# Performance work log

Hardware: AMD Instinct MI355X
Metric: run time of the kernel (lower is better)

## Reference

```python
import jax, jax.numpy as jnp
import numpy as np
import math

N_TOTAL = 262144
C = 128
B = 512
LMAX = 512  # max segment length (static for jit)


def setup_inputs() -> dict:
    key = jax.random.key(0)
    ks = jax.random.split(key, 8)
    Q_feature = jax.random.normal(ks[0], (N_TOTAL, C), dtype=jnp.float32)
    K_feature = jax.random.normal(ks[1], (N_TOTAL, C), dtype=jnp.float32)
    # cumulative offsets: equal segments of length LMAX (general code handles ragged)
    offset = (jnp.arange(1, B + 1, dtype=jnp.int64) * (N_TOTAL // B))
    s = 1.0 / math.sqrt(C)
    Wq = jax.random.normal(ks[2], (C, C), dtype=jnp.float32) * s
    Wk = jax.random.normal(ks[3], (C, C), dtype=jnp.float32) * s
    Wv = jax.random.normal(ks[4], (C, C), dtype=jnp.float32) * s
    bq = jnp.zeros((C,), dtype=jnp.float32)
    bk = jnp.zeros((C,), dtype=jnp.float32)
    bv = jnp.zeros((C,), dtype=jnp.float32)
    return {"Q_feature": Q_feature, "K_feature": K_feature,
            "Wq": Wq, "bq": bq, "Wk": Wk, "bk": bk, "Wv": Wv, "bv": bv,
            "offset": offset}


def reference(Q_feature, K_feature, Wq, bq, Wk, bk, Wv, bv, offset):
    N, Cdim = Q_feature.shape
    Q = Q_feature @ Wq.T + bq
    K = K_feature @ Wk.T + bk
    V = K_feature @ Wv.T + bv

    starts = jnp.concatenate([jnp.zeros((1,), offset.dtype), offset[:-1]])
    lengths = offset - starts                         # (B,)
    pos = jnp.arange(LMAX)                            # (LMAX,)
    idx = jnp.clip(starts[:, None] + pos[None, :], 0, N - 1)  # (B, LMAX)
    mask = pos[None, :] < lengths[:, None]            # (B, LMAX) valid tokens

    Qp = Q[idx]                                       # (B, LMAX, C)
    Kp = K[idx]
    Vp = V[idx]

    scale = 1.0 / math.sqrt(Cdim)
    scores = jnp.einsum('blc,bmc->blm', Qp, Kp) * scale     # (B, LMAX, LMAX)
    scores = jnp.where(mask[:, None, :], scores, jnp.float32(-1e30))
    attn = jax.nn.softmax(scores, axis=-1)
    outp = jnp.einsum('blm,bmc->blc', attn, Vp)             # (B, LMAX, C)
    outp = outp * mask[:, :, None]                          # zero padded rows

    # scatter padded segments back to flat (N, C); idx is an exact partition on valid rows
    out = jnp.zeros((N, Cdim), dtype=outp.dtype).at[idx].add(outp)
    return out
```

## Files before the change

### kernel.cpp

```cpp
#include <hip/hip_runtime.h>
#include <hip/hip_bf16.h>

#define CDIM 128
#define LMAXC 512
#define QBLK 128
#define KVBLK 64

#define QSCALE (0.08838834764831845f * 1.4426950408889634f)

typedef __attribute__((ext_vector_type(8))) short bf16x8;
typedef __attribute__((ext_vector_type(4))) short bf16x4;
typedef __attribute__((ext_vector_type(4))) float f32x4;

__device__ inline short f2bf(float f) {
    union { float f; unsigned u; } v; v.f = f;
    unsigned r = v.u + 0x7FFFu + ((v.u >> 16) & 1u);
    return (short)(r >> 16);
}

__device__ inline bf16x8 cvt8v(float4 a, float4 b) {
    bf16x8 o;
    o[0] = f2bf(a.x); o[1] = f2bf(a.y); o[2] = f2bf(a.z); o[3] = f2bf(a.w);
    o[4] = f2bf(b.x); o[5] = f2bf(b.y); o[6] = f2bf(b.z); o[7] = f2bf(b.w);
    return o;
}

__device__ inline unsigned pk2(float lo, float hi) {
    unsigned r;
    asm("v_cvt_pk_bf16_f32 %0, %1, %2" : "=v"(r) : "v"(lo), "v"(hi));
    return r;
}

__device__ inline void gload16(const void* g, void* l) {
    __builtin_amdgcn_global_load_lds(
        (const __attribute__((address_space(1))) unsigned*)g,
        (__attribute__((address_space(3))) unsigned*)l, 16, 0, 0);
}

__device__ inline void blk_barrier() {
    __builtin_amdgcn_sched_barrier(0);
    __builtin_amdgcn_s_barrier();
    __builtin_amdgcn_sched_barrier(0);
}

__device__ inline int pch(int q) { return ((q + (q >> 3)) & 7) << 4; }

__global__ void wcvt_kernel(const float* __restrict__ Wq,
                            const float* __restrict__ Wk,
                            const float* __restrict__ Wv,
                            short* __restrict__ Wbf)
{
    int t = blockIdx.x * 256 + threadIdx.x;
    int m = t / 2048;
    int e = (t % 2048) * 8;
    const float* W = (m == 0) ? Wq : (m == 1) ? Wk : Wv;
    float sc = (m == 0) ? QSCALE : 1.0f;
    float4 a = *reinterpret_cast<const float4*>(W + e);
    float4 b = *reinterpret_cast<const float4*>(W + e + 4);
    a.x *= sc; a.y *= sc; a.z *= sc; a.w *= sc;
    b.x *= sc; b.y *= sc; b.z *= sc; b.w *= sc;
    *reinterpret_cast<bf16x8*>(Wbf + m * 16384 + e) = cvt8v(a, b);
}

__device__ inline void tile_qk(const char* __restrict__ wlds,
                               const bf16x8 xfr[2][4],
                               const float* __restrict__ bias, float bsc,
                               short* __restrict__ outp, int rowb,
                               int lrow, int lhalf)
{
#pragma unroll
    for (int cf = 0; cf < 8; ++cf) {
        const int key = cf * 16 + lrow;
        bf16x8 wfr[4];
#pragma unroll
        for (int ks = 0; ks < 4; ++ks) {
            int wb = (key * 256 + (ks * 32 + lhalf * 8) * 2) ^ ((key & 7) << 4);
            wfr[ks] = *reinterpret_cast<const bf16x8*>(wlds + wb);
        }
        float4 bv4 = *reinterpret_cast<const float4*>(bias + cf * 16 + lhalf * 4);
#pragma unroll
        for (int xt = 0; xt < 2; ++xt) {
            f32x4 acc = {0.f, 0.f, 0.f, 0.f};
#pragma unroll
            for (int ks = 0; ks < 4; ++ks)
                acc = __builtin_amdgcn_mfma_f32_16x16x32_bf16(wfr[ks], xfr[xt][ks], acc, 0, 0, 0);
            bf16x4 pk;
            pk[0] = f2bf(acc[0] + bv4.x * bsc);
            pk[1] = f2bf(acc[1] + bv4.y * bsc);
            pk[2] = f2bf(acc[2] + bv4.z * bsc);
            pk[3] = f2bf(acc[3] + bv4.w * bsc);
            *reinterpret_cast<bf16x4*>(
                outp + (size_t)(rowb + xt * 16 + lrow) * CDIM
                     + cf * 16 + lhalf * 4) = pk;
        }
    }
}

__device__ inline void tile_v(const char* __restrict__ wlds,
                              const bf16x8 xfr[2][4],
                              const float* __restrict__ bv,
                              short* __restrict__ Vt, int rowb, int N,
                              int lrow, int lhalf)
{
#pragma unroll
    for (int cf = 0; cf < 8; ++cf) {
        const int d = cf * 16 + lrow;
        bf16x8 wfr[4];
#pragma unroll
        for (int ks = 0; ks < 4; ++ks) {
            int wb = (d * 256 + (ks * 32 + lhalf * 8) * 2) ^ ((d & 7) << 4);
            wfr[ks] = *reinterpret_cast<const bf16x8*>(wlds + wb);
        }
        f32x4 acc0 = {0.f, 0.f, 0.f, 0.f};
        f32x4 acc1 = {0.f, 0.f, 0.f, 0.f};
#pragma unroll
        for (int ks = 0; ks < 4; ++ks) {
            acc0 = __builtin_amdgcn_mfma_f32_16x16x32_bf16(xfr[0][ks], wfr[ks], acc0, 0, 0, 0);
            acc1 = __builtin_amdgcn_mfma_f32_16x16x32_bf16(xfr[1][ks], wfr[ks], acc1, 0, 0, 0);
        }
        float bcol = bv[d];
        bf16x4 p0, p1;
#pragma unroll
        for (int r = 0; r < 4; ++r) {
            p0[r] = f2bf(acc0[r] + bcol);
            p1[r] = f2bf(acc1[r] + bcol);
        }
        short* vrow = Vt + (size_t)d * N + rowb + lhalf * 4;
        *reinterpret_cast<bf16x4*>(vrow)      = p0;
        *reinterpret_cast<bf16x4*>(vrow + 16) = p1;
    }
}

__global__ __launch_bounds__(512) void projkv_kernel(
    const float* __restrict__ Kf, const short* __restrict__ Wbf,
    const float* __restrict__ bk, const float* __restrict__ bv,
    short* __restrict__ Kp, short* __restrict__ Vt, int N)
{
    __shared__ __align__(16) char wlds[32768];

    const int tid   = threadIdx.x;
    const int lane  = tid & 63;
    const int wv    = tid >> 6;
    const int lrow  = lane & 15;
    const int lhalf = lane >> 4;
    const int rowb  = blockIdx.x * 256 + wv * 32;

#pragma unroll
    for (int j = 0; j < 4; ++j) {
        int beta = j * 8192 + tid * 16;
        int r  = beta >> 8;
        int gs = ((beta >> 4) & 15) ^ (r & 7);
        gload16(Wbf + 16384 + r * 128 + gs * 8, wlds + beta);
    }

    bf16x8 xfr[2][4];
#pragma unroll
    for (int xt = 0; xt < 2; ++xt) {
        const float* xr = Kf + (size_t)(rowb + xt * 16 + lrow) * CDIM + lhalf * 8;
#pragma unroll
        for (int ks = 0; ks < 4; ++ks) {
            const float4* s = reinterpret_cast<const float4*>(xr + ks * 32);
            xfr[xt][ks] = cvt8v(s[0], s[1]);
        }
    }
    __syncthreads();

    tile_qk(wlds, xfr, bk, 1.0f, Kp, rowb, lrow, lhalf);
    __syncthreads();
#pragma unroll
    for (int j = 0; j < 4; ++j) {
        int beta = j * 8192 + tid * 16;
        int r  = beta >> 8;
        int gs = ((beta >> 4) & 15) ^ (r & 7);
        gload16(Wbf + 32768 + r * 128 + gs * 8, wlds + beta);
    }
    __syncthreads();
    tile_v(wlds, xfr, bv, Vt, rowb, N, lrow, lhalf);
}

__global__ __launch_bounds__(256) void attn_kernel(
    const float* __restrict__ Qf, const short* __restrict__ Wbf,
    const float* __restrict__ bq,
    const short* __restrict__ Kp, const short* __restrict__ VtG,
    const int* __restrict__ offset, float* __restrict__ out, int Ntot)
{
    __shared__ __align__(16) char smem[81920];
    char* lds_p = smem + 65536;

    const int nq = LMAXC / QBLK;
    int flat = blockIdx.x, total = gridDim.x;
    int seg, qb;
    if ((total & (8 * nq - 1)) == 0) {
        int per = total >> 3;
        int xcd = flat & 7;
        int wi  = flat >> 3;
        int sl  = wi / nq;
        qb  = wi - sl * nq;
        seg = xcd * (per / nq) + sl;
    } else { seg = flat / nq; qb = flat - seg * nq; }

    const int start = (seg == 0) ? 0 : offset[seg - 1];
    int len = offset[seg] - start;
    if (len > LMAXC) len = LMAXC;
    const int q0 = qb * QBLK;
    if (q0 >= len) return;

    const int tid   = threadIdx.x;
    const int lane  = tid & 63;
    const int wv    = tid >> 6;
    const int lrow  = lane & 15;
    const int lhalf = lane >> 4;
    const int ntiles = (len + KVBLK - 1) / KVBLK;
    const int lm1 = len - 1;

    auto stage = [&](int kv0, int bb) {
        char* kb = smem + bb * 32768;
        char* vb = kb + 16384;
#pragma unroll
        for (int j = 0; j < 4; ++j) {
            int beta = j * 4096 + wv * 1024 + (lane << 4);
            int r  = beta >> 8;
            int gs = ((beta >> 4) & 15) ^ (r & 7);
            int rg = kv0 + r; if (rg > lm1) rg = lm1;
            gload16(Kp + (((size_t)(start + rg)) << 7) + (gs << 3),
                    kb + j * 4096 + wv * 1024);
            int d   = beta >> 7;
            int gs2 = ((beta >> 4) & 7) ^ (d & 7);
            long gk = (long)start + kv0 + (gs2 << 3);
            if (gk + 8 > Ntot) gk = Ntot - 8;
            gload16(VtG + (size_t)d * Ntot + gk,
                    vb + j * 4096 + wv * 1024);
        }
    };

    stage(0, 0);

    bf16x8 aq[2][4];
    {
        char* qstage = smem + 32768 + wv * 8192;

        bf16x8 xq[2][4];
#pragma unroll
        for (int qt = 0; qt < 2; ++qt) {
            int qr = q0 + wv * 32 + qt * 16 + lrow;
            if (qr > lm1) qr = lm1;
            const float* xr = Qf + (size_t)(start + qr) * CDIM + lhalf * 8;
#pragma unroll
            for (int ks = 0; ks < 4; ++ks) {
                const float4* s = reinterpret_cast<const float4*>(xr + ks * 32);
                xq[qt][ks] = cvt8v(s[0], s[1]);
            }
        }
#pragma unroll
        for (int cf = 0; cf < 8; ++cf) {
            const int key = cf * 16 + lrow;
            bf16x8 wfr[4];
#pragma unroll
            for (int ks = 0; ks < 4; ++ks)
                wfr[ks] = *reinterpret_cast<const bf16x8*>(
                    Wbf + key * CDIM + ks * 32 + lhalf * 8);
            float4 bq4 = *reinterpret_cast<const float4*>(bq + cf * 16 + lhalf * 4);
#pragma unroll
            for (int qt = 0; qt < 2; ++qt) {
                f32x4 acc = {0.f, 0.f, 0.f, 0.f};
#pragma unroll
                for (int ks = 0; ks < 4; ++ks)
                    acc = __builtin_amdgcn_mfma_f32_16x16x32_bf16(wfr[ks], xq[qt][ks], acc, 0, 0, 0);
                bf16x4 pk;
                pk[0] = f2bf(acc[0] + bq4.x * QSCALE);
                pk[1] = f2bf(acc[1] + bq4.y * QSCALE);
                pk[2] = f2bf(acc[2] + bq4.z * QSCALE);
                pk[3] = f2bf(acc[3] + bq4.w * QSCALE);
                int ql = qt * 16 + lrow;
                *reinterpret_cast<bf16x4*>(
                    qstage + ql * 256 + ((cf * 32 + lhalf * 8) ^ pch(ql))) = pk;
            }
        }
        asm volatile("s_waitcnt lgkmcnt(0)" ::: "memory");
        __builtin_amdgcn_sched_barrier(0);
#pragma unroll
        for (int qt = 0; qt < 2; ++qt) {
            int ql = qt * 16 + lrow;
#pragma unroll
            for (int ks = 0; ks < 4; ++ks)
                aq[qt][ks] = *reinterpret_cast<const bf16x8*>(
                    qstage + ql * 256 + ((ks * 64 + lhalf * 16) ^ pch(ql)));
        }
    }
    __syncthreads();

    f32x4 acc_o[2][8];
    float lsum[2] = {0.f, 0.f};
#pragma unroll
    for (int qt = 0; qt < 2; ++qt)
#pragma unroll
        for (int df = 0; df < 8; ++df) acc_o[qt][df] = (f32x4){0.f, 0.f, 0.f, 0.f};

    const int wbase = wv * 4096;

    for (int t = 0; t < ntiles; ++t) {
        const int kv0 = t * KVBLK;
        const int bb  = t & 1;
        if (t + 1 < ntiles) {
            stage(kv0 + KVBLK, bb ^ 1);
            asm volatile("s_waitcnt vmcnt(8)" ::: "memory");
        } else {
            asm volatile("s_waitcnt vmcnt(0)" ::: "memory");
        }
        blk_barrier();

        char* lds_k  = smem + bb * 32768;
        char* lds_vt = lds_k + 16384;
        const bool tail = (kv0 + KVBLK > len);

        f32x4 s0[4], s1[4];
        __builtin_amdgcn_s_setprio(1);
#pragma unroll
        for (int kf = 0; kf < 4; ++kf) {
            s0[kf] = (f32x4){0.f, 0.f, 0.f, 0.f};
            s1[kf] = (f32x4){0.f, 0.f, 0.f, 0.f};
            int key = kf * 16 + lrow;
#pragma unroll
            for (int ks = 0; ks < 4; ++ks) {
                int kbo = (key * 256 + (ks * 32 + lhalf * 8) * 2) ^ ((key & 7) << 4);
                bf16x8 kfr = *reinterpret_cast<const bf16x8*>(lds_k + kbo);
                s0[kf] = __builtin_amdgcn_mfma_f32_16x16x32_bf16(kfr, aq[0][ks], s0[kf], 0, 0, 0);
                s1[kf] = __builtin_amdgcn_mfma_f32_16x16x32_bf16(kfr, aq[1][ks], s1[kf], 0, 0, 0);
            }
        }
        __builtin_amdgcn_s_setprio(0);

        const int keyb0 = kv0 + lhalf * 4;
#pragma unroll
        for (int qt = 0; qt < 2; ++qt) {
            const int qlocal = qt * 16 + lrow;
            const int rowoff = wbase + qlocal * 128;
            const int swz = pch(qlocal);
#pragma unroll
            for (int kf = 0; kf < 4; ++kf) {
                f32x4 sv = qt ? s1[kf] : s0[kf];
                float p[4];
#pragma unroll
                for (int r = 0; r < 4; ++r) {
                    float pv = exp2f(sv[r]);
                    if (tail && (keyb0 + kf * 16 + r >= len)) pv = 0.f;
                    p[r] = pv;
                    lsum[qt] += pv;
                }
                unsigned long long w =
                    (unsigned long long)pk2(p[0], p[1]) |
                    ((unsigned long long)pk2(p[2], p[3]) << 32);
                *reinterpret_cast<unsigned long long*>(
                    lds_p + rowoff + ((kf * 32 + lhalf * 8) ^ swz)) = w;
            }
        }

        __builtin_amdgcn_s_setprio(1);
#pragma unroll
        for (int ks2 = 0; ks2 < 2; ++ks2) {
            bf16x8 ap0 = *reinterpret_cast<const bf16x8*>(
                lds_p + wbase + lrow * 128 + ((ks2 * 64 + lhalf * 16) ^ pch(lrow)));
            bf16x8 ap1 = *reinterpret_cast<const bf16x8*>(
                lds_p + wbase + (16 + lrow) * 128 + ((ks2 * 64 + lhalf * 16) ^ pch(16 + lrow)));
            int k0 = ks2 * 32 + lhalf * 8;
#pragma unroll
            for (int df = 0; df < 8; ++df) {
                int d = df * 16 + lrow;
                int vb2 = (d * 128 + k0 * 2) ^ ((d & 7) << 4);
                bf16x8 bvf = *reinterpret_cast<const bf16x8*>(lds_vt + vb2);
                acc_o[0][df] = __builtin_amdgcn_mfma_f32_16x16x32_bf16(ap0, bvf, acc_o[0][df], 0, 0, 0);
                acc_o[1][df] = __builtin_amdgcn_mfma_f32_16x16x32_bf16(ap1, bvf, acc_o[1][df], 0, 0, 0);
            }
        }
        __builtin_amdgcn_s_setprio(0);

        blk_barrier();
    }

#pragma unroll
    for (int qt = 0; qt < 2; ++qt) {
        float l = lsum[qt];
        l += __shfl_xor(l, 16);
        l += __shfl_xor(l, 32);
        float rinv[4];
#pragma unroll
        for (int r = 0; r < 4; ++r)
            rinv[r] = 1.0f / __shfl(l, lhalf * 4 + r);
#pragma unroll
        for (int df = 0; df < 8; ++df)
#pragma unroll
            for (int r = 0; r < 4; ++r) {
                int qg = q0 + wv * 32 + qt * 16 + lhalf * 4 + r;
                if (qg < len)
                    out[(size_t)(start + qg) * CDIM + df * 16 + lrow]
                        = acc_o[qt][df][r] * rinv[r];
            }
    }
}

extern "C" void kernel_launch(void* const* d_in, const int* in_sizes, int n_in,
                              void* d_out, int out_size, void* d_ws, size_t ws_size,
                              hipStream_t stream) {
    const float* Qf = (const float*)d_in[0];
    const float* Kf = (const float*)d_in[1];
    const float* Wq = (const float*)d_in[2];
    const float* bq = (const float*)d_in[3];
    const float* Wk = (const float*)d_in[4];
    const float* bk = (const float*)d_in[5];
    const float* Wv = (const float*)d_in[6];
    const float* bv_ = (const float*)d_in[7];
    const int* offset = (const int*)d_in[8];

    const int N = in_sizes[0] / CDIM;
    const int B = in_sizes[8];

    short* Kp  = (short*)d_ws;
    short* Vt  = Kp + (size_t)N * CDIM;
    short* Wbf = Vt + (size_t)N * CDIM;
    float* out = (float*)d_out;

    wcvt_kernel<<<24, 256, 0, stream>>>(Wq, Wk, Wv, Wbf);

    projkv_kernel<<<dim3(N / 256), 512, 0, stream>>>(Kf, Wbf, bk, bv_,
                                                     Kp, Vt, N);

    attn_kernel<<<dim3(B * (LMAXC / QBLK)), 256, 0, stream>>>(
        Qf, Wbf, bq, Kp, Vt, offset, out, N);
}
```

Before: 237.1 us.

## Read K and V fragments directly from global memory instead of LDS staging

Removes the double-buffered LDS staging of K and V tiles and the block barriers, so each wave loads its K and V MFMA fragments straight from global memory. LDS shrinks to a per-wave Q/P staging area, which may raise occupancy. The softmax row sum is now taken with an extra MFMA against a vector of ones instead of scalar adds and shuffles. In exchange, the four waves in a block no longer share K/V loads, so global and L2 traffic rises and the loads sit on the critical path with no prefetch.

```diff
diff --git a/kernel.cpp b/kernel.cpp
--- a/kernel.cpp
+++ b/kernel.cpp
@@ -35,12 +35,6 @@
     __builtin_amdgcn_global_load_lds(
         (const __attribute__((address_space(1))) unsigned*)g,
         (__attribute__((address_space(3))) unsigned*)l, 16, 0, 0);
-}
-
-__device__ inline void blk_barrier() {
-    __builtin_amdgcn_sched_barrier(0);
-    __builtin_amdgcn_s_barrier();
-    __builtin_amdgcn_sched_barrier(0);
 }
 
 __device__ inline int pch(int q) { return ((q + (q >> 3)) & 7) << 4; }
@@ -184,8 +178,7 @@
     const short* __restrict__ Kp, const short* __restrict__ VtG,
     const int* __restrict__ offset, float* __restrict__ out, int Ntot)
 {
-    __shared__ __align__(16) char smem[81920];
-    char* lds_p = smem + 65536;
+    __shared__ __align__(16) char smem[32768];
 
     const int nq = LMAXC / QBLK;
     int flat = blockIdx.x, total = gridDim.x;
@@ -213,32 +206,11 @@
     const int ntiles = (len + KVBLK - 1) / KVBLK;
     const int lm1 = len - 1;
 
-    auto stage = [&](int kv0, int bb) {
-        char* kb = smem + bb * 32768;
-        char* vb = kb + 16384;
-#pragma unroll
-        for (int j = 0; j < 4; ++j) {
-            int beta = j * 4096 + wv * 1024 + (lane << 4);
-            int r  = beta >> 8;
-            int gs = ((beta >> 4) & 15) ^ (r & 7);
-            int rg = kv0 + r; if (rg > lm1) rg = lm1;
-            gload16(Kp + (((size_t)(start + rg)) << 7) + (gs << 3),
-                    kb + j * 4096 + wv * 1024);
-            int d   = beta >> 7;
-            int gs2 = ((beta >> 4) & 7) ^ (d & 7);
-            long gk = (long)start + kv0 + (gs2 << 3);
-            if (gk + 8 > Ntot) gk = Ntot - 8;
-            gload16(VtG + (size_t)d * Ntot + gk,
-                    vb + j * 4096 + wv * 1024);
-        }
-    };
-
-    stage(0, 0);
+    char* qstage = smem + wv * 8192;
+    char* pbase  = qstage;
 
     bf16x8 aq[2][4];
     {
-        char* qstage = smem + 32768 + wv * 8192;
-
         bf16x8 xq[2][4];
 #pragma unroll
         for (int qt = 0; qt < 2; ++qt) {
@@ -286,31 +258,26 @@
                 aq[qt][ks] = *reinterpret_cast<const bf16x8*>(
                     qstage + ql * 256 + ((ks * 64 + lhalf * 16) ^ pch(ql)));
         }
-    }
-    __syncthreads();
+        asm volatile("s_waitcnt lgkmcnt(0)" ::: "memory");
+        __builtin_amdgcn_sched_barrier(0);
+    }
 
     f32x4 acc_o[2][8];
-    float lsum[2] = {0.f, 0.f};
+    f32x4 acc_l[2] = {(f32x4){0.f, 0.f, 0.f, 0.f}, (f32x4){0.f, 0.f, 0.f, 0.f}};
 #pragma unroll
     for (int qt = 0; qt < 2; ++qt)
 #pragma unroll
         for (int df = 0; df < 8; ++df) acc_o[qt][df] = (f32x4){0.f, 0.f, 0.f, 0.f};
 
-    const int wbase = wv * 4096;
+    bf16x8 ones;
+#pragma unroll
+    for (int e = 0; e < 8; ++e) ones[e] = (short)0x3F80;
+
+    const short* Ks = Kp + ((size_t)start << 7);
+    const short* Vs = VtG + start;
 
     for (int t = 0; t < ntiles; ++t) {
         const int kv0 = t * KVBLK;
-        const int bb  = t & 1;
-        if (t + 1 < ntiles) {
-            stage(kv0 + KVBLK, bb ^ 1);
-            asm volatile("s_waitcnt vmcnt(8)" ::: "memory");
-        } else {
-            asm volatile("s_waitcnt vmcnt(0)" ::: "memory");
-        }
-        blk_barrier();
-
-        char* lds_k  = smem + bb * 32768;
-        char* lds_vt = lds_k + 16384;
         const bool tail = (kv0 + KVBLK > len);
 
         f32x4 s0[4], s1[4];
@@ -319,11 +286,12 @@
         for (int kf = 0; kf < 4; ++kf) {
             s0[kf] = (f32x4){0.f, 0.f, 0.f, 0.f};
             s1[kf] = (f32x4){0.f, 0.f, 0.f, 0.f};
-            int key = kf * 16 + lrow;
+            int rg = kv0 + kf * 16 + lrow;
+            if (rg > lm1) rg = lm1;
+            const short* krow = Ks + ((size_t)rg << 7) + lhalf * 8;
 #pragma unroll
             for (int ks = 0; ks < 4; ++ks) {
-                int kbo = (key * 256 + (ks * 32 + lhalf * 8) * 2) ^ ((key & 7) << 4);
-                bf16x8 kfr = *reinterpret_cast<const bf16x8*>(lds_k + kbo);
+                bf16x8 kfr = *reinterpret_cast<const bf16x8*>(krow + ks * 32);
                 s0[kf] = __builtin_amdgcn_mfma_f32_16x16x32_bf16(kfr, aq[0][ks], s0[kf], 0, 0, 0);
                 s1[kf] = __builtin_amdgcn_mfma_f32_16x16x32_bf16(kfr, aq[1][ks], s1[kf], 0, 0, 0);
             }
@@ -334,7 +302,7 @@
 #pragma unroll
         for (int qt = 0; qt < 2; ++qt) {
             const int qlocal = qt * 16 + lrow;
-            const int rowoff = wbase + qlocal * 128;
+            const int rowoff = qlocal * 128;
             const int swz = pch(qlocal);
 #pragma unroll
             for (int kf = 0; kf < 4; ++kf) {
@@ -345,13 +313,12 @@
                     float pv = exp2f(sv[r]);
                     if (tail && (keyb0 + kf * 16 + r >= len)) pv = 0.f;
                     p[r] = pv;
-                    lsum[qt] += pv;
                 }
                 unsigned long long w =
                     (unsigned long long)pk2(p[0], p[1]) |
                     ((unsigned long long)pk2(p[2], p[3]) << 32);
                 *reinterpret_cast<unsigned long long*>(
-                    lds_p + rowoff + ((kf * 32 + lhalf * 8) ^ swz)) = w;
+                    pbase + rowoff + ((kf * 32 + lhalf * 8) ^ swz)) = w;
             }
         }
 
@@ -359,33 +326,33 @@
 #pragma unroll
         for (int ks2 = 0; ks2 < 2; ++ks2) {
             bf16x8 ap0 = *reinterpret_cast<const bf16x8*>(
-                lds_p + wbase + lrow * 128 + ((ks2 * 64 + lhalf * 16) ^ pch(lrow)));
+                pbase + lrow * 128 + ((ks2 * 64 + lhalf * 16) ^ pch(lrow)));
             bf16x8 ap1 = *reinterpret_cast<const bf16x8*>(
-                lds_p + wbase + (16 + lrow) * 128 + ((ks2 * 64 + lhalf * 16) ^ pch(16 + lrow)));
-            int k0 = ks2 * 32 + lhalf * 8;
+                pbase + (16 + lrow) * 128 + ((ks2 * 64 + lhalf * 16) ^ pch(16 + lrow)));
+            acc_l[0] = __builtin_amdgcn_mfma_f32_16x16x32_bf16(ap0, ones, acc_l[0], 0, 0, 0);
+            acc_l[1] = __builtin_amdgcn_mfma_f32_16x16x32_bf16(ap1, ones, acc_l[1], 0, 0, 0);
+            const int k0 = kv0 + ks2 * 32 + lhalf * 8;
 #pragma unroll
             for (int df = 0; df < 8; ++df) {
                 int d = df * 16 + lrow;
-                int vb2 = (d * 128 + k0 * 2) ^ ((d & 7) << 4);
-                bf16x8 bvf = *reinterpret_cast<const bf16x8*>(lds_vt + vb2);
+                long gk = k0;
+                if (tail && (size_t)(start + gk + 8) > (size_t)Ntot)
+                    gk = (long)Ntot - start - 8;
+                bf16x8 bvf = *reinterpret_cast<const bf16x8*>(
+                    Vs + (size_t)d * Ntot + gk);
                 acc_o[0][df] = __builtin_amdgcn_mfma_f32_16x16x32_bf16(ap0, bvf, acc_o[0][df], 0, 0, 0);
                 acc_o[1][df] = __builtin_amdgcn_mfma_f32_16x16x32_bf16(ap1, bvf, acc_o[1][df], 0, 0, 0);
             }
         }
         __builtin_amdgcn_s_setprio(0);
-
-        blk_barrier();
     }
 
 #pragma unroll
     for (int qt = 0; qt < 2; ++qt) {
-        float l = lsum[qt];
-        l += __shfl_xor(l, 16);
-        l += __shfl_xor(l, 32);
         float rinv[4];
 #pragma unroll
         for (int r = 0; r < 4; ++r)
-            rinv[r] = 1.0f / __shfl(l, lhalf * 4 + r);
+            rinv[r] = 1.0f / acc_l[qt][r];
 #pragma unroll
         for (int df = 0; df < 8; ++df)
 #pragma unroll
```

Measured after the change: 474.1 us. +100.0%, slower.
